# Optimization experiments

Hardware: AMD Instinct MI355X
Metric: run time of the kernel (lower is better)

Reference implementation:

```python
import jax, jax.numpy as jnp
import numpy as np

SEQ = 2048
HID = 1024
NH = 16
HD = HID // NH


def setup_inputs() -> dict:
    key = jax.random.key(0)
    ks = jax.random.split(key, 5)
    s = 0.02
    return {
        "hidden_states": jax.random.normal(ks[0], (SEQ, HID), dtype=jnp.float32),
        "w_attn": jax.random.normal(ks[1], (HID, 3 * HID), dtype=jnp.float32) * s,
        "b_attn": jax.random.normal(ks[2], (3 * HID,), dtype=jnp.float32) * s,
        "w_proj": jax.random.normal(ks[3], (HID, HID), dtype=jnp.float32) * s,
        "b_proj": jax.random.normal(ks[4], (HID,), dtype=jnp.float32) * s,
    }


def reference(hidden_states, w_attn, b_attn, w_proj, b_proj):
    S = hidden_states.shape[0]
    qkv = hidden_states @ w_attn + b_attn          # [S, 3H]
    q, k, v = jnp.split(qkv, 3, axis=-1)
    q = q.reshape(S, NH, HD)
    k = k.reshape(S, NH, HD)
    v = v.reshape(S, NH, HD)
    sm_scale = 1.0 / np.sqrt(HD).astype(np.float32)
    # explicit scores [h, q, k] in fp32, as in the torch module
    scores = jnp.einsum('qhd,khd->hqk', q.astype(jnp.float32), k.astype(jnp.float32))
    scores = scores * sm_scale
    causal = jnp.tril(jnp.ones((S, S), dtype=bool))  # [q, k]
    scores = jnp.where(causal[None, :, :], scores, -jnp.inf)
    probs = jax.nn.softmax(scores, axis=-1)
    attn = jnp.einsum('hqk,khd->qhd', probs, v.astype(jnp.float32))  # [S, NH, HD]
    attn = attn.reshape(S, HID).astype(hidden_states.dtype)
    return attn @ w_proj + b_proj
```

## Files before the change

kernel.cpp:

```cpp
#include <hip/hip_runtime.h>
#include <cstdint>
#include <cstddef>

#define SEQ 2048
#define HID 1024
#define NHEAD 16
#define HDIM 64

typedef _Float16 f16;
typedef f16 half8 __attribute__((ext_vector_type(8)));
typedef f16 half4 __attribute__((ext_vector_type(4)));
typedef f16 half2_ __attribute__((ext_vector_type(2)));
typedef float f32x4 __attribute__((ext_vector_type(4)));

#define ASYNC_COPY16(g, l)                                                    \
  __builtin_amdgcn_global_load_lds(                                           \
      (const __attribute__((address_space(1))) void*)(const void*)(g),        \
      (__attribute__((address_space(3))) void*)(void*)(l), 16, 0, 0)

__global__ void cast_f32_f16(const float* __restrict__ src,
                             f16* __restrict__ dst, int n) {
  int i = (blockIdx.x * blockDim.x + threadIdx.x) * 4;
  if (i < n) {
    float4 v = *(const float4*)(src + i);
    half4 h;
    h[0] = (f16)v.x; h[1] = (f16)v.y; h[2] = (f16)v.z; h[3] = (f16)v.w;
    *(half4*)(dst + i) = h;
  }
}

__global__ void transpose_cast(const float* __restrict__ src,
                               f16* __restrict__ dst, int R, int C) {
  __shared__ float tile[32][33];
  int c0 = blockIdx.x * 32, r0 = blockIdx.y * 32;
  int tx = threadIdx.x, ty = threadIdx.y;
#pragma unroll
  for (int i = 0; i < 32; i += 8)
    tile[ty + i][tx] = src[(size_t)(r0 + ty + i) * C + c0 + tx];
  __syncthreads();
#pragma unroll
  for (int i = 0; i < 32; i += 8)
    dst[(size_t)(c0 + ty + i) * R + r0 + tx] = (f16)tile[tx][ty + i];
}

template <int BM, int BN, bool OUT16>
__global__ __launch_bounds__(256) void gemm_f16(
    const f16* __restrict__ A, const f16* __restrict__ Bt,
    const float* __restrict__ bias, void* __restrict__ Cout, int M, int N,
    int K) {
  constexpr int FM = BM / 32, FN = BN / 32;
  __shared__ __align__(16) f16 sA[BM * 32];
  __shared__ __align__(16) f16 sB[BN * 32];
  const int tid = threadIdx.x;
  const int wave = tid >> 6, lane = tid & 63;
  const int quad = lane >> 4, l16 = lane & 15;
  const int m0 = blockIdx.y * BM, n0 = blockIdx.x * BN;
  const int wm = (wave >> 1) * (BM / 2), wn = (wave & 1) * (BN / 2);
  const int rowA = lane >> 2, chunkA = lane & 3;

  f32x4 acc[FM][FN] = {};

  for (int k0 = 0; k0 < K; k0 += 32) {
#pragma unroll
    for (int r = wave; r < BM / 16; r += 4)
      ASYNC_COPY16(A + (size_t)(m0 + r * 16 + rowA) * K + k0 + chunkA * 8,
                   &sA[r * 512]);
#pragma unroll
    for (int r = wave; r < BN / 16; r += 4)
      ASYNC_COPY16(Bt + (size_t)(n0 + r * 16 + rowA) * K + k0 + chunkA * 8,
                   &sB[r * 512]);
    __syncthreads();

    half8 af[FM], bf[FN];
#pragma unroll
    for (int i = 0; i < FM; i++)
      af[i] = *(const half8*)&sA[(wm + i * 16 + l16) * 32 + quad * 8];
#pragma unroll
    for (int j = 0; j < FN; j++)
      bf[j] = *(const half8*)&sB[(wn + j * 16 + l16) * 32 + quad * 8];
#pragma unroll
    for (int i = 0; i < FM; i++)
#pragma unroll
      for (int j = 0; j < FN; j++)
        acc[i][j] = __builtin_amdgcn_mfma_f32_16x16x32_f16(af[i], bf[j],
                                                           acc[i][j], 0, 0, 0);
    __syncthreads();
  }

#pragma unroll
  for (int i = 0; i < FM; i++) {
    int row = m0 + wm + i * 16 + quad * 4;
#pragma unroll
    for (int j = 0; j < FN; j++) {
      int col = n0 + wn + j * 16 + l16;
      float bv = bias[col];
#pragma unroll
      for (int r = 0; r < 4; r++) {
        float v = acc[i][j][r] + bv;
        if (OUT16)
          ((f16*)Cout)[(size_t)(row + r) * N + col] = (f16)v;
        else
          ((float*)Cout)[(size_t)(row + r) * N + col] = v;
      }
    }
  }
}

#define LROW 72
#define KROW 72
__global__ __launch_bounds__(256) void attn_split(
    const f16* __restrict__ qkv, f16* __restrict__ out,
    f16* __restrict__ Opart, float* __restrict__ ml) {
  const int b = blockIdx.x;
  const int h = b / 80;
  const int rr_ = b % 80;
  int qt, c, nc;
  if (rr_ < 8)       { qt = rr_;                   c = 0;              nc = 1; }
  else if (rr_ < 24) { qt = 8 + ((rr_ - 8) >> 1);  c = (rr_ - 8) & 1;  nc = 2; }
  else if (rr_ < 48) { qt = 16 + (rr_ - 24) / 3;   c = (rr_ - 24) % 3; nc = 3; }
  else               { qt = 24 + ((rr_ - 48) >> 2); c = (rr_ - 48) & 3; nc = 4; }
  const int q0 = qt * 64;
  const int kt0 = c * 8;
  const int kt1 = (kt0 + 8 < qt + 1) ? kt0 + 8 : qt + 1;

  __shared__ __align__(16) f16 sK[64 * LROW];
  __shared__ __align__(16) f16 sVt[64 * LROW];
  __shared__ __align__(16) f16 sP[4][16 * KROW];

  const int tid = threadIdx.x;
  const int wave = tid >> 6, lane = tid & 63;
  const int quad = lane >> 4, l16 = lane & 15;

  const f16* qbase =
      qkv + (size_t)(q0 + wave * 16 + l16) * 3072 + h * HDIM + quad * 8;
  half8 qf0 = *(const half8*)qbase;
  half8 qf1 = *(const half8*)(qbase + 32);
  const f16 qs = (f16)0.18033688f;
#pragma unroll
  for (int j = 0; j < 8; j++) { qf0[j] *= qs; qf1[j] *= qs; }

  const f16* kbase = qkv + HID + h * HDIM;
  const f16* vbase = qkv + 2 * HID + h * HDIM;

  const int ks_row = tid >> 3, ks_cc = tid & 7;
  const int vs_d = tid & 63, vs_g = tid >> 6;

  f32x4 o[4] = {};
  float m_i = -1e30f, l_i = 0.f;
  half8 kreg[2], vreg[2];

  auto prefetch = [&](int kt) {
    const int k0 = kt * 64;
#pragma unroll
    for (int i = 0; i < 2; i++) {
      kreg[i] = *(const half8*)(kbase + (size_t)(k0 + ks_row + i * 32) * 3072 +
                                ks_cc * 8);
      half8 col;
#pragma unroll
      for (int j = 0; j < 8; j++)
        col[j] = vbase[(size_t)(k0 + (vs_g + i * 4) * 8 + j) * 3072 + vs_d];
      vreg[i] = col;
    }
  };

  prefetch(kt0);
  for (int kt = kt0; kt < kt1; kt++) {
    const int k0 = kt * 64;
#pragma unroll
    for (int i = 0; i < 2; i++) {
      *(half8*)&sK[(ks_row + i * 32) * LROW + ks_cc * 8] = kreg[i];
      *(half8*)&sVt[vs_d * LROW + (vs_g + i * 4) * 8] = vreg[i];
    }
    __syncthreads();
    if (kt + 1 < kt1) prefetch(kt + 1);

    f32x4 sacc[4] = {};
#pragma unroll
    for (int kb = 0; kb < 4; kb++) {
      half8 kf0 = *(const half8*)&sK[(kb * 16 + l16) * LROW + quad * 8];
      half8 kf1 = *(const half8*)&sK[(kb * 16 + l16) * LROW + 32 + quad * 8];
      sacc[kb] =
          __builtin_amdgcn_mfma_f32_16x16x32_f16(kf0, qf0, sacc[kb], 0, 0, 0);
      sacc[kb] =
          __builtin_amdgcn_mfma_f32_16x16x32_f16(kf1, qf1, sacc[kb], 0, 0, 0);
    }
    if (kt == qt) {
      const int qg = q0 + wave * 16 + l16;
#pragma unroll
      for (int kb = 0; kb < 4; kb++) {
        int kg = k0 + kb * 16 + quad * 4;
#pragma unroll
        for (int r = 0; r < 4; r++)
          if (kg + r > qg) sacc[kb][r] = -1e30f;
      }
    }
    float mx = -1e30f;
#pragma unroll
    for (int kb = 0; kb < 4; kb++)
#pragma unroll
      for (int r = 0; r < 4; r++) mx = fmaxf(mx, sacc[kb][r]);
    mx = fmaxf(mx, __shfl_xor(mx, 16));
    mx = fmaxf(mx, __shfl_xor(mx, 32));
    const float mnew = fmaxf(m_i, mx);
    const float alpha = exp2f(m_i - mnew);
    float rs = 0.f;
#pragma unroll
    for (int kb = 0; kb < 4; kb++)
#pragma unroll
      for (int r = 0; r < 4; r++) {
        float p = exp2f(sacc[kb][r] - mnew);
        sacc[kb][r] = p;
        rs += p;
      }
    rs += __shfl_xor(rs, 16);
    rs += __shfl_xor(rs, 32);
    l_i = l_i * alpha + rs;
    m_i = mnew;
#pragma unroll
    for (int j = 0; j < 4; j++)
#pragma unroll
      for (int r = 0; r < 4; r++) o[j][r] *= alpha;

    f16* pw = &sP[wave][l16 * KROW];
#pragma unroll
    for (int kb = 0; kb < 4; kb++)
#pragma unroll
      for (int rp = 0; rp < 2; rp++) {
        half2_ pv;
        pv[0] = (f16)sacc[kb][rp * 2];
        pv[1] = (f16)sacc[kb][rp * 2 + 1];
        *(half2_*)&pw[kb * 16 + quad * 4 + rp * 2] = pv;
      }
    half8 pf0 = *(const half8*)&pw[quad * 8];
    half8 pf1 = *(const half8*)&pw[32 + quad * 8];
#pragma unroll
    for (int j = 0; j < 4; j++) {
      half8 vf0 = *(const half8*)&sVt[(j * 16 + l16) * LROW + quad * 8];
      half8 vf1 = *(const half8*)&sVt[(j * 16 + l16) * LROW + 32 + quad * 8];
      o[j] = __builtin_amdgcn_mfma_f32_16x16x32_f16(vf0, pf0, o[j], 0, 0, 0);
      o[j] = __builtin_amdgcn_mfma_f32_16x16x32_f16(vf1, pf1, o[j], 0, 0, 0);
    }
    __syncthreads();
  }

  if (nc == 1) {
    const float inv = 1.f / l_i;
    f16* orow = out + (size_t)(q0 + wave * 16 + l16) * HID + h * HDIM;
#pragma unroll
    for (int j = 0; j < 4; j++) {
      half4 hv;
#pragma unroll
      for (int r = 0; r < 4; r++) hv[r] = (f16)(o[j][r] * inv);
      *(half4*)&orow[j * 16 + quad * 4] = hv;
    }
  } else {
    int base;
    if (qt < 16)      base = (qt - 8) * 2 + c;
    else if (qt < 24) base = 16 + (qt - 16) * 3 + c;
    else              base = 40 + (qt - 24) * 4 + c;
    const int slot = h * 72 + base;
    f16* op = Opart + (size_t)slot * 4096 + (wave * 16 + l16) * 64;
#pragma unroll
    for (int j = 0; j < 4; j++) {
      half4 hv;
#pragma unroll
      for (int r = 0; r < 4; r++) hv[r] = (f16)o[j][r];
      *(half4*)&op[j * 16 + quad * 4] = hv;
    }
    if (quad == 0) {
      ml[slot * 128 + wave * 16 + l16] = m_i;
      ml[slot * 128 + 64 + wave * 16 + l16] = l_i;
    }
  }
}

__global__ __launch_bounds__(256) void attn_combine(
    const f16* __restrict__ Opart, const float* __restrict__ ml,
    f16* __restrict__ out) {
  int idx = blockIdx.x * 256 + threadIdx.x;
  int d = idx & 63;
  int r64 = (idx >> 6) & 63;
  int rest = idx >> 12;
  int qtl = rest % 24;
  int h = rest / 24;
  int qt = 8 + qtl;
  int g = qtl >> 3, i = qtl & 7;
  int nc = g + 2;
  int base = (g == 0) ? i * 2 : (g == 1) ? 16 + i * 3 : 40 + i * 4;
  int slot0 = h * 72 + base;

  float m[4], l[4];
  float M = -1e30f;
  for (int cc = 0; cc < nc; cc++) {
    m[cc] = ml[(slot0 + cc) * 128 + r64];
    l[cc] = ml[(slot0 + cc) * 128 + 64 + r64];
    M = fmaxf(M, m[cc]);
  }
  float L = 0.f, acc = 0.f;
  for (int cc = 0; cc < nc; cc++) {
    float w = exp2f(m[cc] - M);
    L += w * l[cc];
    acc += w * (float)Opart[(size_t)(slot0 + cc) * 4096 + r64 * 64 + d];
  }
  out[(size_t)(qt * 64 + r64) * HID + h * HDIM + d] = (f16)(acc / L);
}

extern "C" void kernel_launch(void* const* d_in, const int* in_sizes, int n_in,
                              void* d_out, int out_size, void* d_ws,
                              size_t ws_size, hipStream_t stream) {
  const float* h = (const float*)d_in[0];
  const float* wa = (const float*)d_in[1];
  const float* ba = (const float*)d_in[2];
  const float* wp = (const float*)d_in[3];
  const float* bp = (const float*)d_in[4];
  float* out = (float*)d_out;

  char* ws = (char*)d_ws;
  f16* h16 = (f16*)(ws);
  f16* waT = (f16*)(ws + (4u << 20));
  f16* wpT = (f16*)(ws + (10u << 20));
  f16* qkv = (f16*)(ws + (12u << 20));
  f16* attn = (f16*)(ws + (24u << 20));
  f16* Opart = (f16*)(ws);
  float* mlbuf = (float*)(ws + 9437184);

  cast_f32_f16<<<2048, 256, 0, stream>>>(h, h16, SEQ * HID);
  transpose_cast<<<dim3(96, 32), dim3(32, 8), 0, stream>>>(wa, waT, 1024, 3072);
  transpose_cast<<<dim3(32, 32), dim3(32, 8), 0, stream>>>(wp, wpT, 1024, 1024);
  gemm_f16<128, 64, true><<<dim3(48, 16), 256, 0, stream>>>(
      h16, waT, ba, qkv, SEQ, 3 * HID, HID);
  attn_split<<<1280, 256, 0, stream>>>(qkv, attn, Opart, mlbuf);
  attn_combine<<<6144, 256, 0, stream>>>(Opart, mlbuf, attn);
  gemm_f16<64, 64, false><<<dim3(16, 32), 256, 0, stream>>>(
      attn, wpT, bp, out, SEQ, HID, HID);
}
```

Before: 166.7 us.

## Use 128-row query tiles in attention, fuse prologue kernels, widen QKV GEMM tile

The attention split kernel now has each wave handle 32 query rows in two 16-row groups, so every block covers 128 queries. Each K/V tile loaded into shared memory is reused across twice as many queries, and the grid halves to 640 blocks with a new split/slot layout and a matching combine kernel. The three cast/transpose prologue kernels are merged into one launch, and the QKV GEMM tile grows to 128x128. The trade-offs are higher register pressure (launch bounds ask for 3 blocks per SM), fewer blocks for load balancing, and more fully-masked work on the diagonal tiles.

Result: faster. 160.5 us (-3.7%).

```diff
diff --git a/kernel.cpp b/kernel.cpp
--- a/kernel.cpp
+++ b/kernel.cpp
@@ -18,29 +18,32 @@
       (const __attribute__((address_space(1))) void*)(const void*)(g),        \
       (__attribute__((address_space(3))) void*)(void*)(l), 16, 0, 0)
 
-__global__ void cast_f32_f16(const float* __restrict__ src,
-                             f16* __restrict__ dst, int n) {
-  int i = (blockIdx.x * blockDim.x + threadIdx.x) * 4;
-  if (i < n) {
-    float4 v = *(const float4*)(src + i);
-    half4 h;
-    h[0] = (f16)v.x; h[1] = (f16)v.y; h[2] = (f16)v.z; h[3] = (f16)v.w;
-    *(half4*)(dst + i) = h;
-  }
-}
-
-__global__ void transpose_cast(const float* __restrict__ src,
-                               f16* __restrict__ dst, int R, int C) {
+__global__ __launch_bounds__(256) void prologue(
+    const float* __restrict__ h, const float* __restrict__ wa,
+    const float* __restrict__ wp, f16* __restrict__ h16,
+    f16* __restrict__ waT, f16* __restrict__ wpT) {
+  const int b = blockIdx.x, tid = threadIdx.x;
+  if (b >= 4096) {
+    int i = ((b - 4096) * 256 + tid) * 4;
+    float4 v = *(const float4*)(h + i);
+    half4 o;
+    o[0] = (f16)v.x; o[1] = (f16)v.y; o[2] = (f16)v.z; o[3] = (f16)v.w;
+    *(half4*)(h16 + i) = o;
+    return;
+  }
+  const float* src; f16* dst; int C, bx, by;
+  if (b < 3072) { src = wa; dst = waT; C = 3072; bx = b % 96; by = b / 96; }
+  else { int t = b - 3072; src = wp; dst = wpT; C = 1024; bx = t & 31; by = t >> 5; }
   __shared__ float tile[32][33];
-  int c0 = blockIdx.x * 32, r0 = blockIdx.y * 32;
-  int tx = threadIdx.x, ty = threadIdx.y;
+  const int tx = tid & 31, ty = tid >> 5;
+  const int c0 = bx * 32, r0 = by * 32;
 #pragma unroll
   for (int i = 0; i < 32; i += 8)
     tile[ty + i][tx] = src[(size_t)(r0 + ty + i) * C + c0 + tx];
   __syncthreads();
 #pragma unroll
   for (int i = 0; i < 32; i += 8)
-    dst[(size_t)(c0 + ty + i) * R + r0 + tx] = (f16)tile[tx][ty + i];
+    dst[(size_t)(c0 + ty + i) * 1024 + r0 + tx] = (f16)tile[tx][ty + i];
 }
 
 template <int BM, int BN, bool OUT16>
@@ -107,46 +110,50 @@
 }
 
 #define LROW 72
-#define KROW 72
-__global__ __launch_bounds__(256) void attn_split(
+__global__ __launch_bounds__(256, 3) void attn_split(
     const f16* __restrict__ qkv, f16* __restrict__ out,
     f16* __restrict__ Opart, float* __restrict__ ml) {
   const int b = blockIdx.x;
-  const int h = b / 80;
-  const int rr_ = b % 80;
-  int qt, c, nc;
-  if (rr_ < 8)       { qt = rr_;                   c = 0;              nc = 1; }
-  else if (rr_ < 24) { qt = 8 + ((rr_ - 8) >> 1);  c = (rr_ - 8) & 1;  nc = 2; }
-  else if (rr_ < 48) { qt = 16 + (rr_ - 24) / 3;   c = (rr_ - 24) % 3; nc = 3; }
-  else               { qt = 24 + ((rr_ - 48) >> 2); c = (rr_ - 48) & 3; nc = 4; }
-  const int q0 = qt * 64;
+  const int h = b / 40;
+  const int t = b % 40;
+  int m, c, nc;
+  if (t < 4)       { m = t;                 c = 0;      nc = 1; }
+  else if (t < 12) { int u = t - 4;  m = 4 + (u >> 1);  c = u & 1; nc = 2; }
+  else if (t < 24) { int u = t - 12; m = 8 + u / 3;     c = u % 3; nc = 3; }
+  else             { int u = t - 24; m = 12 + (u >> 2); c = u & 3; nc = 4; }
+  const int q0 = m * 128;
+  const int T = 2 * m + 2;
   const int kt0 = c * 8;
-  const int kt1 = (kt0 + 8 < qt + 1) ? kt0 + 8 : qt + 1;
+  const int kt1 = (kt0 + 8 < T) ? kt0 + 8 : T;
+  const int maskFrom = 2 * m;
 
   __shared__ __align__(16) f16 sK[64 * LROW];
   __shared__ __align__(16) f16 sVt[64 * LROW];
-  __shared__ __align__(16) f16 sP[4][16 * KROW];
+  __shared__ __align__(16) f16 sP[4][32 * LROW];
 
   const int tid = threadIdx.x;
   const int wave = tid >> 6, lane = tid & 63;
   const int quad = lane >> 4, l16 = lane & 15;
 
-  const f16* qbase =
-      qkv + (size_t)(q0 + wave * 16 + l16) * 3072 + h * HDIM + quad * 8;
-  half8 qf0 = *(const half8*)qbase;
-  half8 qf1 = *(const half8*)(qbase + 32);
   const f16 qs = (f16)0.18033688f;
-#pragma unroll
-  for (int j = 0; j < 8; j++) { qf0[j] *= qs; qf1[j] *= qs; }
+  half8 qf[2][2];
+#pragma unroll
+  for (int g = 0; g < 2; g++) {
+    const f16* qb = qkv + (size_t)(q0 + wave * 32 + g * 16 + l16) * 3072 +
+                    h * HDIM + quad * 8;
+    qf[g][0] = *(const half8*)qb;
+    qf[g][1] = *(const half8*)(qb + 32);
+#pragma unroll
+    for (int j = 0; j < 8; j++) { qf[g][0][j] *= qs; qf[g][1][j] *= qs; }
+  }
 
   const f16* kbase = qkv + HID + h * HDIM;
   const f16* vbase = qkv + 2 * HID + h * HDIM;
-
   const int ks_row = tid >> 3, ks_cc = tid & 7;
   const int vs_d = tid & 63, vs_g = tid >> 6;
 
-  f32x4 o[4] = {};
-  float m_i = -1e30f, l_i = 0.f;
+  f32x4 o[2][4] = {};
+  float m_i[2] = {-1e30f, -1e30f}, l_i[2] = {0.f, 0.f};
   half8 kreg[2], vreg[2];
 
   auto prefetch = [&](int kt) {
@@ -174,102 +181,122 @@
     __syncthreads();
     if (kt + 1 < kt1) prefetch(kt + 1);
 
-    f32x4 sacc[4] = {};
+    f32x4 sacc[2][4] = {};
 #pragma unroll
     for (int kb = 0; kb < 4; kb++) {
       half8 kf0 = *(const half8*)&sK[(kb * 16 + l16) * LROW + quad * 8];
       half8 kf1 = *(const half8*)&sK[(kb * 16 + l16) * LROW + 32 + quad * 8];
-      sacc[kb] =
-          __builtin_amdgcn_mfma_f32_16x16x32_f16(kf0, qf0, sacc[kb], 0, 0, 0);
-      sacc[kb] =
-          __builtin_amdgcn_mfma_f32_16x16x32_f16(kf1, qf1, sacc[kb], 0, 0, 0);
-    }
-    if (kt == qt) {
-      const int qg = q0 + wave * 16 + l16;
-#pragma unroll
-      for (int kb = 0; kb < 4; kb++) {
-        int kg = k0 + kb * 16 + quad * 4;
-#pragma unroll
-        for (int r = 0; r < 4; r++)
-          if (kg + r > qg) sacc[kb][r] = -1e30f;
-      }
-    }
-    float mx = -1e30f;
-#pragma unroll
-    for (int kb = 0; kb < 4; kb++)
-#pragma unroll
-      for (int r = 0; r < 4; r++) mx = fmaxf(mx, sacc[kb][r]);
-    mx = fmaxf(mx, __shfl_xor(mx, 16));
-    mx = fmaxf(mx, __shfl_xor(mx, 32));
-    const float mnew = fmaxf(m_i, mx);
-    const float alpha = exp2f(m_i - mnew);
-    float rs = 0.f;
-#pragma unroll
-    for (int kb = 0; kb < 4; kb++)
-#pragma unroll
-      for (int r = 0; r < 4; r++) {
-        float p = exp2f(sacc[kb][r] - mnew);
-        sacc[kb][r] = p;
-        rs += p;
-      }
-    rs += __shfl_xor(rs, 16);
-    rs += __shfl_xor(rs, 32);
-    l_i = l_i * alpha + rs;
-    m_i = mnew;
-#pragma unroll
-    for (int j = 0; j < 4; j++)
-#pragma unroll
-      for (int r = 0; r < 4; r++) o[j][r] *= alpha;
-
-    f16* pw = &sP[wave][l16 * KROW];
-#pragma unroll
-    for (int kb = 0; kb < 4; kb++)
-#pragma unroll
-      for (int rp = 0; rp < 2; rp++) {
-        half2_ pv;
-        pv[0] = (f16)sacc[kb][rp * 2];
-        pv[1] = (f16)sacc[kb][rp * 2 + 1];
-        *(half2_*)&pw[kb * 16 + quad * 4 + rp * 2] = pv;
-      }
-    half8 pf0 = *(const half8*)&pw[quad * 8];
-    half8 pf1 = *(const half8*)&pw[32 + quad * 8];
+#pragma unroll
+      for (int g = 0; g < 2; g++) {
+        sacc[g][kb] = __builtin_amdgcn_mfma_f32_16x16x32_f16(kf0, qf[g][0],
+                                                             sacc[g][kb], 0, 0, 0);
+        sacc[g][kb] = __builtin_amdgcn_mfma_f32_16x16x32_f16(kf1, qf[g][1],
+                                                             sacc[g][kb], 0, 0, 0);
+      }
+    }
+    if (kt >= maskFrom) {
+#pragma unroll
+      for (int g = 0; g < 2; g++) {
+        const int qg = q0 + wave * 32 + g * 16 + l16;
+#pragma unroll
+        for (int kb = 0; kb < 4; kb++) {
+          int kg = k0 + kb * 16 + quad * 4;
+#pragma unroll
+          for (int r = 0; r < 4; r++)
+            if (kg + r > qg) sacc[g][kb][r] = -1e30f;
+        }
+      }
+    }
+#pragma unroll
+    for (int g = 0; g < 2; g++) {
+      float mx = -1e30f;
+#pragma unroll
+      for (int kb = 0; kb < 4; kb++)
+#pragma unroll
+        for (int r = 0; r < 4; r++) mx = fmaxf(mx, sacc[g][kb][r]);
+      mx = fmaxf(mx, __shfl_xor(mx, 16));
+      mx = fmaxf(mx, __shfl_xor(mx, 32));
+      const float mnew = fmaxf(m_i[g], mx);
+      const float alpha = exp2f(m_i[g] - mnew);
+      float rs = 0.f;
+#pragma unroll
+      for (int kb = 0; kb < 4; kb++)
+#pragma unroll
+        for (int r = 0; r < 4; r++) {
+          float p = exp2f(sacc[g][kb][r] - mnew);
+          sacc[g][kb][r] = p;
+          rs += p;
+        }
+      rs += __shfl_xor(rs, 16);
+      rs += __shfl_xor(rs, 32);
+      l_i[g] = l_i[g] * alpha + rs;
+      m_i[g] = mnew;
+#pragma unroll
+      for (int j = 0; j < 4; j++)
+#pragma unroll
+        for (int r = 0; r < 4; r++) o[g][j][r] *= alpha;
+      f16* pw = &sP[wave][(g * 16 + l16) * LROW];
+#pragma unroll
+      for (int kb = 0; kb < 4; kb++)
+#pragma unroll
+        for (int rp = 0; rp < 2; rp++) {
+          half2_ pv;
+          pv[0] = (f16)sacc[g][kb][rp * 2];
+          pv[1] = (f16)sacc[g][kb][rp * 2 + 1];
+          *(half2_*)&pw[kb * 16 + quad * 4 + rp * 2] = pv;
+        }
+    }
 #pragma unroll
     for (int j = 0; j < 4; j++) {
       half8 vf0 = *(const half8*)&sVt[(j * 16 + l16) * LROW + quad * 8];
       half8 vf1 = *(const half8*)&sVt[(j * 16 + l16) * LROW + 32 + quad * 8];
-      o[j] = __builtin_amdgcn_mfma_f32_16x16x32_f16(vf0, pf0, o[j], 0, 0, 0);
-      o[j] = __builtin_amdgcn_mfma_f32_16x16x32_f16(vf1, pf1, o[j], 0, 0, 0);
+#pragma unroll
+      for (int g = 0; g < 2; g++) {
+        half8 pf0 = *(const half8*)&sP[wave][(g * 16 + l16) * LROW + quad * 8];
+        half8 pf1 =
+            *(const half8*)&sP[wave][(g * 16 + l16) * LROW + 32 + quad * 8];
+        o[g][j] = __builtin_amdgcn_mfma_f32_16x16x32_f16(vf0, pf0, o[g][j], 0, 0, 0);
+        o[g][j] = __builtin_amdgcn_mfma_f32_16x16x32_f16(vf1, pf1, o[g][j], 0, 0, 0);
+      }
     }
     __syncthreads();
   }
 
   if (nc == 1) {
-    const float inv = 1.f / l_i;
-    f16* orow = out + (size_t)(q0 + wave * 16 + l16) * HID + h * HDIM;
-#pragma unroll
-    for (int j = 0; j < 4; j++) {
-      half4 hv;
-#pragma unroll
-      for (int r = 0; r < 4; r++) hv[r] = (f16)(o[j][r] * inv);
-      *(half4*)&orow[j * 16 + quad * 4] = hv;
+#pragma unroll
+    for (int g = 0; g < 2; g++) {
+      const float inv = 1.f / l_i[g];
+      f16* orow =
+          out + (size_t)(q0 + wave * 32 + g * 16 + l16) * HID + h * HDIM;
+#pragma unroll
+      for (int j = 0; j < 4; j++) {
+        half4 hv;
+#pragma unroll
+        for (int r = 0; r < 4; r++) hv[r] = (f16)(o[g][j][r] * inv);
+        *(half4*)&orow[j * 16 + quad * 4] = hv;
+      }
     }
   } else {
     int base;
-    if (qt < 16)      base = (qt - 8) * 2 + c;
-    else if (qt < 24) base = 16 + (qt - 16) * 3 + c;
-    else              base = 40 + (qt - 24) * 4 + c;
-    const int slot = h * 72 + base;
-    f16* op = Opart + (size_t)slot * 4096 + (wave * 16 + l16) * 64;
-#pragma unroll
-    for (int j = 0; j < 4; j++) {
-      half4 hv;
-#pragma unroll
-      for (int r = 0; r < 4; r++) hv[r] = (f16)o[j][r];
-      *(half4*)&op[j * 16 + quad * 4] = hv;
-    }
-    if (quad == 0) {
-      ml[slot * 128 + wave * 16 + l16] = m_i;
-      ml[slot * 128 + 64 + wave * 16 + l16] = l_i;
+    if (m < 8)       base = (m - 4) * 2;
+    else if (m < 12) base = 8 + (m - 8) * 3;
+    else             base = 20 + (m - 12) * 4;
+    const int slot = h * 36 + base + c;
+#pragma unroll
+    for (int g = 0; g < 2; g++) {
+      const int qrow = wave * 32 + g * 16 + l16;
+      f16* op = Opart + (size_t)slot * 8192 + qrow * 64;
+#pragma unroll
+      for (int j = 0; j < 4; j++) {
+        half4 hv;
+#pragma unroll
+        for (int r = 0; r < 4; r++) hv[r] = (f16)o[g][j][r];
+        *(half4*)&op[j * 16 + quad * 4] = hv;
+      }
+      if (quad == 0) {
+        ml[slot * 256 + qrow] = m_i[g];
+        ml[slot * 256 + 128 + qrow] = l_i[g];
+      }
     }
   }
 }
@@ -279,30 +306,29 @@
     f16* __restrict__ out) {
   int idx = blockIdx.x * 256 + threadIdx.x;
   int d = idx & 63;
-  int r64 = (idx >> 6) & 63;
-  int rest = idx >> 12;
-  int qtl = rest % 24;
-  int h = rest / 24;
-  int qt = 8 + qtl;
-  int g = qtl >> 3, i = qtl & 7;
-  int nc = g + 2;
-  int base = (g == 0) ? i * 2 : (g == 1) ? 16 + i * 3 : 40 + i * 4;
-  int slot0 = h * 72 + base;
-
-  float m[4], l[4];
+  int row = (idx >> 6) & 127;
+  int rest = idx >> 13;
+  int mi = rest % 12;
+  int h = rest / 12;
+  int m = 4 + mi;
+  int nc = (mi < 4) ? 2 : (mi < 8) ? 3 : 4;
+  int base = (mi < 4) ? mi * 2 : (mi < 8) ? 8 + (mi - 4) * 3 : 20 + (mi - 8) * 4;
+  int slot0 = h * 36 + base;
+
+  float mm[4], ll[4];
   float M = -1e30f;
   for (int cc = 0; cc < nc; cc++) {
-    m[cc] = ml[(slot0 + cc) * 128 + r64];
-    l[cc] = ml[(slot0 + cc) * 128 + 64 + r64];
-    M = fmaxf(M, m[cc]);
+    mm[cc] = ml[(slot0 + cc) * 256 + row];
+    ll[cc] = ml[(slot0 + cc) * 256 + 128 + row];
+    M = fmaxf(M, mm[cc]);
   }
   float L = 0.f, acc = 0.f;
   for (int cc = 0; cc < nc; cc++) {
-    float w = exp2f(m[cc] - M);
-    L += w * l[cc];
-    acc += w * (float)Opart[(size_t)(slot0 + cc) * 4096 + r64 * 64 + d];
-  }
-  out[(size_t)(qt * 64 + r64) * HID + h * HDIM + d] = (f16)(acc / L);
+    float w = exp2f(mm[cc] - M);
+    L += w * ll[cc];
+    acc += w * (float)Opart[(size_t)(slot0 + cc) * 8192 + row * 64 + d];
+  }
+  out[(size_t)(m * 128 + row) * HID + h * HDIM + d] = (f16)(acc / L);
 }
 
 extern "C" void kernel_launch(void* const* d_in, const int* in_sizes, int n_in,
@@ -324,12 +350,10 @@
   f16* Opart = (f16*)(ws);
   float* mlbuf = (float*)(ws + 9437184);
 
-  cast_f32_f16<<<2048, 256, 0, stream>>>(h, h16, SEQ * HID);
-  transpose_cast<<<dim3(96, 32), dim3(32, 8), 0, stream>>>(wa, waT, 1024, 3072);
-  transpose_cast<<<dim3(32, 32), dim3(32, 8), 0, stream>>>(wp, wpT, 1024, 1024);
-  gemm_f16<128, 64, true><<<dim3(48, 16), 256, 0, stream>>>(
+  prologue<<<6144, 256, 0, stream>>>(h, wa, wp, h16, waT, wpT);
+  gemm_f16<128, 128, true><<<dim3(24, 16), 256, 0, stream>>>(
       h16, waT, ba, qkv, SEQ, 3 * HID, HID);
-  attn_split<<<1280, 256, 0, stream>>>(qkv, attn, Opart, mlbuf);
+  attn_split<<<640, 256, 0, stream>>>(qkv, attn, Opart, mlbuf);
   attn_combine<<<6144, 256, 0, stream>>>(Opart, mlbuf, attn);
   gemm_f16<64, 64, false><<<dim3(16, 32), 256, 0, stream>>>(
       attn, wpT, bp, out, SEQ, HID, HID);
```
